# Kernel tuning notes

Measured on AMD Instinct MI355X. Metric: run time of the kernel, lower is better.

Reference implementation:

```python
import jax, jax.numpy as jnp
import numpy as np

_LOG2PI = float(np.log(2.0 * np.pi))


def setup_inputs() -> dict:
    key = jax.random.key(0)
    ks = jax.random.split(key, 9)
    B, T, S, A, O = 64, 128, 512, 16, 4096
    regime = jax.random.randint(ks[0], (B,), 0, 2).astype(jnp.float32)
    obs = jax.random.randint(ks[1], (T + 1, B), 0, O, dtype=jnp.int32)
    rewards = jax.random.normal(ks[2], (T + 1, B), jnp.float32)
    dones = jnp.zeros((T + 1, B), jnp.float32)
    actions = jax.random.randint(ks[3], (T, B), 0, A, dtype=jnp.int32)
    prior_logits = jax.random.normal(ks[4], (S,), jnp.float32)
    trans_logits = jax.random.normal(ks[5], (A, S, S), jnp.float32)
    obs_logits = jax.random.normal(ks[6], (S, O), jnp.float32)
    policy_logits = jax.random.normal(ks[7], (S, A), jnp.float32)
    r_mu = jax.random.normal(ks[8], (S,), jnp.float32)
    r_logsig = jnp.zeros((S,), jnp.float32)
    return {"regime": regime, "obs": obs, "rewards": rewards, "dones": dones,
            "actions": actions, "prior_logits": prior_logits,
            "trans_logits": trans_logits, "obs_logits": obs_logits,
            "policy_logits": policy_logits, "r_mu": r_mu, "r_logsig": r_logsig}


def _log_prob(regime, obs, rewards, dones, actions, prior_logits, trans_logits,
              obs_logits, policy_logits, r_mu, r_logsig):
    # normalized log-prob tables (tabular instantiation of AugmentedModel)
    log_prior = jax.nn.log_softmax(prior_logits)              # [S]
    log_trans = jax.nn.log_softmax(trans_logits, axis=-1)     # [A,S,S]
    log_obs = jax.nn.log_softmax(obs_logits, axis=-1)         # [S,O]
    log_pol = jax.nn.log_softmax(policy_logits, axis=-1)      # [S,A]
    lse = jax.scipy.special.logsumexp

    def emis(o, r):  # log q(o|s) + log q(r|s) -> [B,S]
        lo = log_obs.T[o]                                      # [B,S] gather
        lr = (-0.5 * (((r[:, None] - r_mu[None, :]) * jnp.exp(-r_logsig)[None, :]) ** 2)
              - r_logsig[None, :] - 0.5 * _LOG2PI)             # [B,S]
        return lo + lr

    def act_term(a, done):  # masked log q(a|s) -> [B,S]
        la = log_pol.T[a]                                      # [B,S]
        la = jnp.where((done == 1.0)[:, None], jnp.zeros_like(la), la)
        la = jnp.where((regime == 1.0)[:, None], jnp.zeros_like(la), la)
        return la

    T = actions.shape[0]
    B = regime.shape[0]

    # t = 0
    was_done = jnp.zeros((B,), rewards.dtype)
    done0 = dones[0]
    lq_sorda = log_prior[None, :] + emis(obs[0], rewards[0]) + act_term(actions[0], done0)
    lq_orda = lse(lq_sorda, axis=-1) * (1.0 - was_done)        # [B]
    log_prob = lq_orda
    lq_s_h = lq_sorda - lq_orda[:, None]
    # belief propagation through transition: [B,S,1] + [B,S,S] -> lse over prev state
    lq_snext_h = lse(lq_s_h[:, :, None] + log_trans[actions[0]], axis=1)

    def step(carry, xs):  # t = 1 .. T-1 (has an action)
        log_prob, was_done, lq_s_hprev = carry
        o, r, d, a = xs
        done = jnp.maximum(was_done, d)
        lq = lq_s_hprev + emis(o, r) + act_term(a, done)
        lq_orda = lse(lq, axis=-1) * (1.0 - was_done)
        log_prob = jnp.where(jnp.isinf(log_prob), log_prob, log_prob + lq_orda)
        lq_s_h = lq - lq_orda[:, None]
        lq_snext = lse(lq_s_h[:, :, None] + log_trans[a], axis=1)
        return (log_prob, done, lq_snext), None

    xs = (obs[1:T], rewards[1:T], dones[1:T], actions[1:T])
    (log_prob, was_done, lq_s_hprev), _ = jax.lax.scan(
        step, (log_prob, done0, lq_snext_h), xs)

    # final step t = T (no action term)
    lq = lq_s_hprev + emis(obs[T], rewards[T])
    lq_ord = lse(lq, axis=-1) * (1.0 - was_done)
    log_prob = jnp.where(jnp.isinf(log_prob), log_prob, log_prob + lq_ord)
    return log_prob


def reference(regime, obs, rewards, dones, actions, prior_logits, trans_logits,
              obs_logits, policy_logits, r_mu, r_logsig):
    return _log_prob(regime, obs, rewards, dones, actions, prior_logits,
                     trans_logits, obs_logits, policy_logits, r_mu, r_logsig)
```

## Files before the change

kernel.cpp:

```cpp
#include <hip/hip_runtime.h>
#include <math.h>

#define DI __device__ __forceinline__

constexpr int BB = 64;
constexpr int TT = 128;
constexpr int SS = 512;
constexpr int AA = 16;
constexpr int OO = 4096;
constexpr float LOG2PI = 1.8378770664093453f;
constexpr float LOG4096 = 8.317766166719343f;

typedef float f32x4 __attribute__((ext_vector_type(4)));

DI void lds_barrier() {
    asm volatile("s_waitcnt lgkmcnt(0)\n\ts_barrier" ::: "memory");
}

typedef __attribute__((address_space(3))) unsigned int as3_u32;
typedef __attribute__((address_space(1))) const unsigned int as1_u32;
DI void dma1k(const unsigned char* g, unsigned char* l) {
    __builtin_amdgcn_global_load_lds((as1_u32*)g, (as3_u32*)l, 16, 0, 0);
}

DI unsigned int f32_to_e4m3(float x) {
    unsigned int u = __float_as_uint(x);
    unsigned int lsb = (u >> 20) & 1u;
    unsigned int rounded = u + 0x7ffffu + lsb;
    int e8 = (int)(rounded >> 23) - 120;
    unsigned int m3 = (rounded >> 20) & 7u;
    unsigned int norm = ((unsigned int)e8 << 3) | m3;
    int sub = __float2int_rn(x * 512.0f);
    return (e8 <= 0) ? (unsigned int)sub : norm;
}

DI float bflyMax(float v) {
#pragma unroll
    for (int off = 32; off; off >>= 1) v = fmaxf(v, __shfl_xor(v, off));
    return v;
}
DI float bflySum(float v) {
#pragma unroll
    for (int off = 32; off; off >>= 1) v += __shfl_xor(v, off);
    return v;
}
DI float halfMax(float v) {
#pragma unroll
    for (int off = 16; off; off >>= 1) v = fmaxf(v, __shfl_xor(v, off));
    return v;
}
DI float halfSum(float v) {
#pragma unroll
    for (int off = 16; off; off >>= 1) v += __shfl_xor(v, off);
    return v;
}

template <int NW>
DI float blockMax(float v, float* wr) {
    v = bflyMax(v);
    const int lane = threadIdx.x & 63, wv = threadIdx.x >> 6;
    if (lane == 0) wr[wv] = v;
    __syncthreads();
    float r = wr[0];
#pragma unroll
    for (int i = 1; i < NW; ++i) r = fmaxf(r, wr[i]);
    __syncthreads();
    return r;
}
template <int NW>
DI float blockSum(float v, float* wr) {
    v = bflySum(v);
    const int lane = threadIdx.x & 63, wv = threadIdx.x >> 6;
    if (lane == 0) wr[wv] = v;
    __syncthreads();
    float r = wr[0];
#pragma unroll
    for (int i = 1; i < NW; ++i) r += wr[i];
    __syncthreads();
    return r;
}


__global__ __launch_bounds__(1024) void k_pack(const float* __restrict__ tl,
                                               unsigned char* __restrict__ PB) {
    __shared__ unsigned char lds[16384];
    const int a = blockIdx.x >> 4;
    const int kt = blockIdx.x & 15;
    const int tid = threadIdx.x;
    const int r = tid >> 5;
    const int nt = tid & 31;
    const int k = kt * 32 + r;
    const float* row = tl + ((size_t)a * SS + k) * SS + nt * 16;

    float x[16];
#pragma unroll
    for (int i = 0; i < 4; ++i) {
        float4 v = ((const float4*)row)[i];
        x[4 * i] = v.x; x[4 * i + 1] = v.y; x[4 * i + 2] = v.z; x[4 * i + 3] = v.w;
    }
    float mx = -INFINITY;
#pragma unroll
    for (int i = 0; i < 16; ++i) mx = fmaxf(mx, x[i]);
    mx = halfMax(mx);
    float e[16];
    float sm = 0.f;
#pragma unroll
    for (int i = 0; i < 16; ++i) { e[i] = __expf(x[i] - mx); sm += e[i]; }
    sm = halfSum(sm);
    const float scale = 256.0f / sm;

    const int base = (nt >> 1) * 1024 + ((r >> 3) * 16) * 16 + (nt & 1) * 8 + (r & 7);
#pragma unroll
    for (int i = 0; i < 16; ++i) {
        lds[base + i * 16] = (unsigned char)f32_to_e4m3(e[i] * scale);
    }
    __syncthreads();

    ulonglong2* dst = (ulonglong2*)(PB + (size_t)(a * 16 + kt) * 16384);
    dst[tid] = ((const ulonglong2*)lds)[tid];
}

__global__ __launch_bounds__(256) void k_obs_stats(const float* __restrict__ ol,
                                                   float* __restrict__ mo,
                                                   float* __restrict__ lo) {
    __shared__ float wr[4];
    const int s = blockIdx.x;
    const float* in = ol + (size_t)s * OO;
    const int tid = threadIdx.x;
    float mx = -INFINITY;
    for (int i = tid; i < OO; i += 256) mx = fmaxf(mx, in[i]);
    float m = blockMax<4>(mx, wr);
    float sm = 0.f;
    for (int i = tid; i < OO; i += 256) sm += __expf(in[i] - m);
    float sum = blockSum<4>(sm, wr);
    if (tid == 0) { mo[s] = m; lo[s] = __logf(sum); }
}

__global__ __launch_bounds__(256) void k_obsT(const float* __restrict__ ol,
                                              const float* __restrict__ mo,
                                              const float* __restrict__ lo,
                                              float* __restrict__ obsT) {
    __shared__ float tile[64][65];
    const int tO = blockIdx.x % (OO / 64);
    const int tS = blockIdx.x / (OO / 64);
    const int o0 = tO * 64, s0 = tS * 64;
    const int cc = threadIdx.x & 63, rr = threadIdx.x >> 6;
#pragma unroll
    for (int j = 0; j < 16; ++j) {
        int r = rr + j * 4;
        tile[r][cc] = ol[(size_t)(s0 + r) * OO + o0 + cc] - mo[s0 + r] - lo[s0 + r];
    }
    __syncthreads();
#pragma unroll
    for (int j = 0; j < 16; ++j) {
        int r = rr + j * 4;
        obsT[(size_t)(o0 + r) * SS + s0 + cc] = tile[cc][r];
    }
}

__global__ __launch_bounds__(512) void k_main(
    const float* __restrict__ regime, const int* __restrict__ obs,
    const float* __restrict__ rewards, const float* __restrict__ dones,
    const int* __restrict__ actions, const float* __restrict__ prior_logits,
    const unsigned char* __restrict__ PB, const float* __restrict__ obsT,
    const float* __restrict__ policy_logits, const float* __restrict__ r_mu,
    const float* __restrict__ r_logsig, float* __restrict__ out) {
    __shared__ unsigned char stage[3 * 16384];
    __shared__ float wrm[8], wrs[8];
    __shared__ unsigned char p8[4 * 144 + 16];
    __shared__ float lqprev[SS];
    __shared__ int obs_l[TT + 1];
    __shared__ float rew_l[TT + 1];
    __shared__ float done_l[TT + 1];
    __shared__ int act_l[TT];

    const int b = blockIdx.x;
    const int tid = threadIdx.x;
    const int wv = tid >> 6, lane = tid & 63, quad = lane >> 4;
    const int s = tid;

    if (tid <= TT) {
        obs_l[tid] = obs[tid * BB + b];
        rew_l[tid] = rewards[tid * BB + b];
        done_l[tid] = dones[tid * BB + b];
        if (tid < TT) act_l[tid] = actions[tid * BB + b];
    }
    float la16[16];
    {
        const float4* pr4 = (const float4*)(policy_logits + (size_t)s * AA);
        float4 v0 = pr4[0], v1 = pr4[1], v2 = pr4[2], v3 = pr4[3];
        la16[0] = v0.x; la16[1] = v0.y; la16[2] = v0.z; la16[3] = v0.w;
        la16[4] = v1.x; la16[5] = v1.y; la16[6] = v1.z; la16[7] = v1.w;
        la16[8] = v2.x; la16[9] = v2.y; la16[10] = v2.z; la16[11] = v2.w;
        la16[12] = v3.x; la16[13] = v3.y; la16[14] = v3.z; la16[15] = v3.w;
        float mx = la16[0];
#pragma unroll
        for (int i = 1; i < 16; ++i) mx = fmaxf(mx, la16[i]);
        float sm = 0.f;
#pragma unroll
        for (int i = 0; i < 16; ++i) sm += __expf(la16[i] - mx);
        float ls = mx + __logf(sm);
#pragma unroll
        for (int i = 0; i < 16; ++i) la16[i] -= ls;
    }
    const float rm = r_mu[s];
    const float rls = r_logsig[s];
    const float inv_sig = __expf(-rls);
    const float reg = regime[b];

    float px = prior_logits[s];
    {
        float wm0 = bflyMax(px);
        if (lane == 0) wrm[wv] = wm0;
    }
    lds_barrier();
    float pm = wrm[0];
#pragma unroll
    for (int i = 1; i < 8; ++i) pm = fmaxf(pm, wrm[i]);
    {
        float ws0 = bflySum(__expf(px - pm));
        if (lane == 0) wrs[wv] = ws0;
    }
    lds_barrier();
    float psum = wrs[0];
#pragma unroll
    for (int i = 1; i < 8; ++i) psum += wrs[i];
    const float prior_reg = px - pm - __logf(psum);

    float obsv = obsT[(size_t)obs_l[0] * SS + s];

    float log_prob = 0.f;
    float was_done = 0.f;

    for (int t = 0; t < TT; ++t) {
        const float r = rew_l[t];
        const int a = __builtin_amdgcn_readfirstlane(act_l[t]);
        const float d = done_l[t];
        const float done = fmaxf(was_done, d);

        const unsigned char* PBa = PB + (size_t)a * (16 * 16384);
        unsigned char* mystage = stage + wv * 2048;

#pragma unroll
        for (int c = 0; c < 3; ++c) {
            const unsigned char* g = PBa + c * 16384 + (2 * wv) * 1024 + lane * 16;
            unsigned char* l = mystage + c * 16384;
            dma1k(g, l);
            dma1k(g + 1024, l + 1024);
        }
        asm volatile("" ::: "memory");
        float obsv_next = obsT[(size_t)obs_l[t + 1] * SS + s];
        asm volatile("" ::: "memory");

        float diff = (r - rm) * inv_sig;
        float emis = obsv - 0.5f * diff * diff - rls - 0.5f * LOG2PI;
        float base_in = (t == 0) ? prior_reg : lqprev[s];
        float la = la16[0];
#pragma unroll
        for (int i = 1; i < 16; ++i) la = (a == i) ? la16[i] : la;
        if (done == 1.0f || reg == 1.0f) la = 0.f;
        float lq = base_in + emis + la;

        float wmax = bflyMax(lq);
        if (lane == 0) wrm[wv] = wmax;
        lds_barrier();
        float m = wrm[0];
#pragma unroll
        for (int i = 1; i < 8; ++i) m = fmaxf(m, wrm[i]);

        float exv = __expf(lq - m);
        p8[((s >> 3) & 3) * 144 + (s >> 5) * 8 + (s & 7)] =
            (unsigned char)f32_to_e4m3(exv * 16.0f);
        float wsum = bflySum(exv);
        if (lane == 0) wrs[wv] = wsum;
        lds_barrier();
        float sum = wrs[0];
#pragma unroll
        for (int i = 1; i < 8; ++i) sum += wrs[i];
        float lse = m + __logf(sum);
        float lq_orda = lse * (1.0f - was_done);
        if (!isinf(log_prob)) log_prob += lq_orda;
        was_done = done;

        const float basev = m - lq_orda - LOG4096;
        f32x4 acc0 = {0.f, 0.f, 0.f, 0.f};
        f32x4 acc1 = {0.f, 0.f, 0.f, 0.f};
        f32x4 acc2 = {0.f, 0.f, 0.f, 0.f};
        f32x4 acc3 = {0.f, 0.f, 0.f, 0.f};

#define CHUNK(c, WN)                                                            \
        {                                                                       \
            asm volatile("s_waitcnt vmcnt(" #WN ")" ::: "memory");              \
            const unsigned char* sb = mystage + ((c) % 3) * 16384 + lane * 16;  \
            ulonglong2 f0 = *(const ulonglong2*)(sb);                           \
            ulonglong2 f1 = *(const ulonglong2*)(sb + 1024);                    \
            long af = *(const long long*)(p8 + quad * 144 + (c) * 8);           \
            acc0 = __builtin_amdgcn_mfma_f32_16x16x32_fp8_fp8((long)f0.x, af, acc0, 0, 0, 0); \
            acc1 = __builtin_amdgcn_mfma_f32_16x16x32_fp8_fp8((long)f0.y, af, acc1, 0, 0, 0); \
            acc2 = __builtin_amdgcn_mfma_f32_16x16x32_fp8_fp8((long)f1.x, af, acc2, 0, 0, 0); \
            acc3 = __builtin_amdgcn_mfma_f32_16x16x32_fp8_fp8((long)f1.y, af, acc3, 0, 0, 0); \
            if ((c) + 3 < 16) {                                                 \
                asm volatile("s_waitcnt lgkmcnt(0)" ::: "memory");              \
                const unsigned char* g = PBa + ((c) + 3) * 16384 + (2 * wv) * 1024 + lane * 16; \
                unsigned char* l = mystage + ((c) % 3) * 16384;                 \
                dma1k(g, l);                                                    \
                dma1k(g + 1024, l + 1024);                                      \
            }                                                                   \
        }
        CHUNK(0, 5)  CHUNK(1, 5)  CHUNK(2, 5)  CHUNK(3, 4)
        CHUNK(4, 4)  CHUNK(5, 4)  CHUNK(6, 4)  CHUNK(7, 4)
        CHUNK(8, 4)  CHUNK(9, 4)  CHUNK(10, 4) CHUNK(11, 4)
        CHUNK(12, 4) CHUNK(13, 4) CHUNK(14, 2) CHUNK(15, 0)
#undef CHUNK

        if (lane < 16) {
            lqprev[wv * 64 + lane]      = basev + __logf(acc0[0]);
            lqprev[wv * 64 + 16 + lane] = basev + __logf(acc1[0]);
            lqprev[wv * 64 + 32 + lane] = basev + __logf(acc2[0]);
            lqprev[wv * 64 + 48 + lane] = basev + __logf(acc3[0]);
        }
        lds_barrier();
        obsv = obsv_next;
    }

    {
        const float r = rew_l[TT];
        float diff = (r - rm) * inv_sig;
        float emis = obsv - 0.5f * diff * diff - rls - 0.5f * LOG2PI;
        float lq = lqprev[s] + emis;
        float wmax = bflyMax(lq);
        if (lane == 0) wrm[wv] = wmax;
        lds_barrier();
        float m = wrm[0];
#pragma unroll
        for (int i = 1; i < 8; ++i) m = fmaxf(m, wrm[i]);
        float wsum = bflySum(__expf(lq - m));
        if (lane == 0) wrs[wv] = wsum;
        lds_barrier();
        float sum = wrs[0];
#pragma unroll
        for (int i = 1; i < 8; ++i) sum += wrs[i];
        float lse = m + __logf(sum);
        float lq_ord = lse * (1.0f - was_done);
        if (!isinf(log_prob)) log_prob += lq_ord;
    }

    if (tid == 0) out[b] = log_prob;
}

extern "C" void kernel_launch(void* const* d_in, const int* in_sizes, int n_in,
                              void* d_out, int out_size, void* d_ws, size_t ws_size,
                              hipStream_t stream) {
    const float* regime = (const float*)d_in[0];
    const int* obs = (const int*)d_in[1];
    const float* rewards = (const float*)d_in[2];
    const float* dones = (const float*)d_in[3];
    const int* actions = (const int*)d_in[4];
    const float* prior_logits = (const float*)d_in[5];
    const float* trans_logits = (const float*)d_in[6];
    const float* obs_logits = (const float*)d_in[7];
    const float* policy_logits = (const float*)d_in[8];
    const float* r_mu = (const float*)d_in[9];
    const float* r_logsig = (const float*)d_in[10];
    float* out = (float*)d_out;

    char* ws = (char*)d_ws;
    unsigned char* PB = (unsigned char*)ws;
    float* obsT = (float*)(ws + (size_t)AA * SS * SS);
    float* mo = (float*)(ws + (size_t)AA * SS * SS + (size_t)OO * SS * 4);
    float* lo = mo + SS;

    k_pack<<<256, 1024, 0, stream>>>(trans_logits, PB);
    k_obs_stats<<<SS, 256, 0, stream>>>(obs_logits, mo, lo);
    k_obsT<<<(OO / 64) * (SS / 64), 256, 0, stream>>>(obs_logits, mo, lo, obsT);
    k_main<<<BB, 512, 0, stream>>>(regime, obs, rewards, dones, actions, prior_logits,
                                   PB, obsT, policy_logits, r_mu, r_logsig, out);
}
```

Measured before the change: 536.8 us.

## Load transition fp8 tiles straight into registers instead of LDS DMA staging

```diff
diff --git a/kernel.cpp b/kernel.cpp
--- a/kernel.cpp
+++ b/kernel.cpp
@@ -15,12 +15,6 @@
 
 DI void lds_barrier() {
     asm volatile("s_waitcnt lgkmcnt(0)\n\ts_barrier" ::: "memory");
-}
-
-typedef __attribute__((address_space(3))) unsigned int as3_u32;
-typedef __attribute__((address_space(1))) const unsigned int as1_u32;
-DI void dma1k(const unsigned char* g, unsigned char* l) {
-    __builtin_amdgcn_global_load_lds((as1_u32*)g, (as3_u32*)l, 16, 0, 0);
 }
 
 DI unsigned int f32_to_e4m3(float x) {
@@ -165,7 +159,6 @@
     const unsigned char* __restrict__ PB, const float* __restrict__ obsT,
     const float* __restrict__ policy_logits, const float* __restrict__ r_mu,
     const float* __restrict__ r_logsig, float* __restrict__ out) {
-    __shared__ unsigned char stage[3 * 16384];
     __shared__ float wrm[8], wrs[8];
     __shared__ unsigned char p8[4 * 144 + 16];
     __shared__ float lqprev[SS];
@@ -238,17 +231,15 @@
         const float d = done_l[t];
         const float done = fmaxf(was_done, d);
 
-        const unsigned char* PBa = PB + (size_t)a * (16 * 16384);
-        unsigned char* mystage = stage + wv * 2048;
-
-#pragma unroll
-        for (int c = 0; c < 3; ++c) {
-            const unsigned char* g = PBa + c * 16384 + (2 * wv) * 1024 + lane * 16;
-            unsigned char* l = mystage + c * 16384;
-            dma1k(g, l);
-            dma1k(g + 1024, l + 1024);
+        const unsigned char* Pw =
+            PB + (size_t)a * (16 * 16384) + (size_t)(wv * 2048 + lane * 16);
+
+        ulonglong2 fA[8], fB[8];
+#pragma unroll
+        for (int c = 0; c < 8; ++c) {
+            fA[c] = *(const ulonglong2*)(Pw + c * 16384);
+            fB[c] = *(const ulonglong2*)(Pw + c * 16384 + 1024);
         }
-        asm volatile("" ::: "memory");
         float obsv_next = obsT[(size_t)obs_l[t + 1] * SS + s];
         asm volatile("" ::: "memory");
 
@@ -288,29 +279,22 @@
         f32x4 acc2 = {0.f, 0.f, 0.f, 0.f};
         f32x4 acc3 = {0.f, 0.f, 0.f, 0.f};
 
-#define CHUNK(c, WN)                                                            \
+#define CHUNK(c)                                                                \
         {                                                                       \
-            asm volatile("s_waitcnt vmcnt(" #WN ")" ::: "memory");              \
-            const unsigned char* sb = mystage + ((c) % 3) * 16384 + lane * 16;  \
-            ulonglong2 f0 = *(const ulonglong2*)(sb);                           \
-            ulonglong2 f1 = *(const ulonglong2*)(sb + 1024);                    \
             long af = *(const long long*)(p8 + quad * 144 + (c) * 8);           \
-            acc0 = __builtin_amdgcn_mfma_f32_16x16x32_fp8_fp8((long)f0.x, af, acc0, 0, 0, 0); \
-            acc1 = __builtin_amdgcn_mfma_f32_16x16x32_fp8_fp8((long)f0.y, af, acc1, 0, 0, 0); \
-            acc2 = __builtin_amdgcn_mfma_f32_16x16x32_fp8_fp8((long)f1.x, af, acc2, 0, 0, 0); \
-            acc3 = __builtin_amdgcn_mfma_f32_16x16x32_fp8_fp8((long)f1.y, af, acc3, 0, 0, 0); \
-            if ((c) + 3 < 16) {                                                 \
-                asm volatile("s_waitcnt lgkmcnt(0)" ::: "memory");              \
-                const unsigned char* g = PBa + ((c) + 3) * 16384 + (2 * wv) * 1024 + lane * 16; \
-                unsigned char* l = mystage + ((c) % 3) * 16384;                 \
-                dma1k(g, l);                                                    \
-                dma1k(g + 1024, l + 1024);                                      \
+            acc0 = __builtin_amdgcn_mfma_f32_16x16x32_fp8_fp8((long)fA[(c) & 7].x, af, acc0, 0, 0, 0); \
+            acc1 = __builtin_amdgcn_mfma_f32_16x16x32_fp8_fp8((long)fA[(c) & 7].y, af, acc1, 0, 0, 0); \
+            acc2 = __builtin_amdgcn_mfma_f32_16x16x32_fp8_fp8((long)fB[(c) & 7].x, af, acc2, 0, 0, 0); \
+            acc3 = __builtin_amdgcn_mfma_f32_16x16x32_fp8_fp8((long)fB[(c) & 7].y, af, acc3, 0, 0, 0); \
+            if ((c) + 8 < 16) {                                                 \
+                fA[(c) & 7] = *(const ulonglong2*)(Pw + ((c) + 8) * 16384);     \
+                fB[(c) & 7] = *(const ulonglong2*)(Pw + ((c) + 8) * 16384 + 1024); \
             }                                                                   \
         }
-        CHUNK(0, 5)  CHUNK(1, 5)  CHUNK(2, 5)  CHUNK(3, 4)
-        CHUNK(4, 4)  CHUNK(5, 4)  CHUNK(6, 4)  CHUNK(7, 4)
-        CHUNK(8, 4)  CHUNK(9, 4)  CHUNK(10, 4) CHUNK(11, 4)
-        CHUNK(12, 4) CHUNK(13, 4) CHUNK(14, 2) CHUNK(15, 0)
+        CHUNK(0)  CHUNK(1)  CHUNK(2)  CHUNK(3)
+        CHUNK(4)  CHUNK(5)  CHUNK(6)  CHUNK(7)
+        CHUNK(8)  CHUNK(9)  CHUNK(10) CHUNK(11)
+        CHUNK(12) CHUNK(13) CHUNK(14) CHUNK(15)
 #undef CHUNK
 
         if (lane < 16) {
@@ -319,7 +303,7 @@
             lqprev[wv * 64 + 32 + lane] = basev + __logf(acc2[0]);
             lqprev[wv * 64 + 48 + lane] = basev + __logf(acc3[0]);
         }
-        lds_barrier();
+        asm volatile("s_waitcnt lgkmcnt(0)" ::: "memory");
         obsv = obsv_next;
     }
 
```

Measured after the change: 492.7 us. 8.2% less time.
